# Kernel tuning notes

Measured on AMD Instinct MI355X. Metric: run time of the kernel, lower is better.

The kernel has to match this reference:

```python
import jax, jax.numpy as jnp
import numpy as np

B, C, D, H, W = 16, 8, 511, 16, 16
NHEADS = 16
DIM = C * H * W          # 2048 hidden size
SEQ = D + 1              # 512 tokens incl. cls
HEAD_DIM = DIM // NHEADS # 128


def setup_inputs() -> dict:
    key = jax.random.key(0)
    ks = jax.random.split(key, 8)
    s = 0.02  # weight init scale
    return {
        "x": jax.random.normal(ks[0], (B, C, D, H, W), jnp.float32),
        "pos_embedding": jax.random.normal(ks[1], (1, SEQ, DIM), jnp.float32),
        "cls": jax.random.normal(ks[2], (1, 1, DIM), jnp.float32),
        "qkv_w": jax.random.normal(ks[3], (DIM, 3 * DIM), jnp.float32) * s,
        "qkv_b": jnp.zeros((3 * DIM,), jnp.float32),
        "proj_w": jax.random.normal(ks[4], (DIM, DIM), jnp.float32) * s,
        "proj_b": jnp.zeros((DIM,), jnp.float32),
    }


def reference(x, pos_embedding, cls, qkv_w, qkv_b, proj_w, proj_b):
    b = x.shape[0]
    # rearrange 'b c d h w -> b d (c h w)'
    tok = jnp.transpose(x, (0, 2, 1, 3, 4)).reshape(b, D, DIM)
    tok = jnp.concatenate([jnp.broadcast_to(cls, (b, 1, DIM)), tok], axis=1)
    tok = tok + pos_embedding  # (b, SEQ, DIM)
    # qkv projection (dropout probs are 0 -> identity)
    qkv = tok @ qkv_w + qkv_b  # (b, SEQ, 3*DIM)
    qkv = qkv.reshape(b, SEQ, 3, NHEADS, HEAD_DIM).transpose(2, 0, 3, 1, 4)
    q, k, v = qkv[0], qkv[1], qkv[2]  # each (b, nH, SEQ, hd)
    scale = HEAD_DIM ** -0.5
    score = jax.nn.softmax(jnp.einsum('bhqd,bhkd->bhqk', q, k) * scale, axis=-1)
    out = jnp.einsum('bhqk,bhkd->bhqd', score, v)
    out = out.transpose(0, 2, 1, 3).reshape(b, SEQ, DIM)
    out = out @ proj_w + proj_b
    return out[:, 0]  # cls token, (b, DIM)
```

## Files before the change

### kernel.cpp

```cpp
#include <hip/hip_runtime.h>


#define BB   16
#define CC   8
#define DD   511
#define DIM  2048
#define SEQ  512
#define NH   16
#define HD   128
#define W3   6144
#define SCALE 0.08838834764831845f

#define Q_OFF   0
#define G_OFF   2048
#define AO_OFF  2064
#define SC_OFF  34832
#define ZERO_N  165904
#define R_OFF   165904
#define RB_OFF  198672
#define U_OFF   231440
#define POST_OFF 755728

#define PSTR 520

typedef __attribute__((ext_vector_type(8))) short short8;
typedef __attribute__((ext_vector_type(4))) float floatx4;

static __device__ inline short bf_hi(float f) {
  return (short)(__float_as_uint(f) >> 16);
}
static __device__ inline float bf_hif(float f) {
  return __uint_as_float(__float_as_uint(f) & 0xffff0000u);
}

__global__ __launch_bounds__(256) void k0_prep(
    const float* __restrict__ pos, float* __restrict__ ws,
    float* __restrict__ out) {
  int blk = blockIdx.x + blockIdx.y * 16;
  int t = threadIdx.x;
  for (int i = blk * 256 + t; i < ZERO_N; i += 1024 * 256) ws[i] = 0.f;
  for (int i = blk * 256 + t; i < BB * DIM; i += 1024 * 256) out[i] = 0.f;
  __shared__ float tile[32][33];
  int jt = blockIdx.x, dt = blockIdx.y;
  int tx = t & 31, ty = t >> 5;
#pragma unroll
  for (int r = 0; r < 32; r += 8)
    tile[ty + r][tx] = pos[(size_t)(jt * 32 + ty + r) * DIM + dt * 32 + tx];
  __syncthreads();
  float* pt = ws + POST_OFF;
#pragma unroll
  for (int r = 0; r < 32; r += 8)
    pt[(size_t)(dt * 32 + ty + r) * SEQ + jt * 32 + tx] = tile[tx][ty + r];
}

__global__ __launch_bounds__(256) void k1_q(
    const float* __restrict__ pos, const float* __restrict__ cls,
    const float* __restrict__ qkv_w, const float* __restrict__ qkv_b,
    float* __restrict__ ws) {
  int n  = blockIdx.x * 256 + threadIdx.x;
  int d0 = blockIdx.y * 32;
  float acc = (blockIdx.y == 0) ? qkv_b[n] : 0.f;
#pragma unroll 8
  for (int d = d0; d < d0 + 32; ++d) {
    float t0 = cls[d] + pos[d];
    acc += t0 * qkv_w[(size_t)d * W3 + n];
  }
  atomicAdd(&ws[Q_OFF + n], acc);
}

__global__ __launch_bounds__(128) void k2_r(
    const float* __restrict__ qkv_w, const float* __restrict__ pos,
    const float* __restrict__ cls, float* __restrict__ ws) {
  __shared__ float qs[HD];
  int h = blockIdx.y;
  int d = blockIdx.x * 128 + threadIdx.x;
  if (threadIdx.x < HD) qs[threadIdx.x] = ws[Q_OFF + h * HD + threadIdx.x];
  __syncthreads();
  const float4* w4 = reinterpret_cast<const float4*>(
      qkv_w + (size_t)d * W3 + DIM + h * HD);
  float acc = 0.f;
#pragma unroll 8
  for (int e4 = 0; e4 < 32; ++e4) {
    float4 w = w4[e4];
    acc += qs[e4*4+0]*w.x + qs[e4*4+1]*w.y + qs[e4*4+2]*w.z + qs[e4*4+3]*w.w;
  }
  float r = acc * SCALE;
  int i = h * DIM + d;
  ws[R_OFF + i] = r;
  short* rb = (short*)(ws + RB_OFF);
  rb[i] = bf_hi(r);
  rb[NH * DIM + i] = bf_hi(r - bf_hif(r));
  float g = (cls[d] + pos[d]) * r;
  for (int m = 1; m < 64; m <<= 1) g += __shfl_xor(g, m, 64);
  if ((threadIdx.x & 63) == 0) atomicAdd(&ws[G_OFF + h], g);
}

__global__ __launch_bounds__(256) void k3_scores_mfma(
    const float* __restrict__ x, const float* __restrict__ pos,
    float* __restrict__ ws) {
  int jt2 = blockIdx.x, b = blockIdx.y, ks = blockIdx.z;
  int t = threadIdx.x;
  int w = t >> 6, l = t & 63;
  int jt = jt2 * 4 + w;
  int m16 = l & 15, kg = l >> 4;
  int jrow = 1 + jt * 16 + m16;
  int jc = jrow < SEQ ? jrow : (SEQ - 1);
  const size_t xrow = (size_t)b * CC * DD * 256 + (size_t)(jc - 1) * 256;
  const short* rh = (const short*)(ws + RB_OFF);
  const short* rl = rh + NH * DIM;
  floatx4 acc = {0.f, 0.f, 0.f, 0.f};
#pragma unroll 2
  for (int kk = ks * 16; kk < ks * 16 + 16; ++kk) {
    int d0 = kk * 32 + kg * 8;
    int c = d0 >> 8, doff = d0 & 255;
    const float4* xp = reinterpret_cast<const float4*>(
        x + xrow + (size_t)c * DD * 256 + doff);
    const float4* pp = reinterpret_cast<const float4*>(
        pos + (size_t)jc * DIM + d0);
    float4 xa = xp[0], xb = xp[1];
    float4 pa = pp[0], pb = pp[1];
    float f[8] = {xa.x + pa.x, xa.y + pa.y, xa.z + pa.z, xa.w + pa.w,
                  xb.x + pb.x, xb.y + pb.y, xb.z + pb.z, xb.w + pb.w};
    short8 ahi, alo;
#pragma unroll
    for (int i = 0; i < 8; ++i) {
      ahi[i] = bf_hi(f[i]);
      alo[i] = bf_hi(f[i] - bf_hif(f[i]));
    }
    short8 bhi = *reinterpret_cast<const short8*>(rh + m16 * DIM + d0);
    short8 blo = *reinterpret_cast<const short8*>(rl + m16 * DIM + d0);
    acc = __builtin_amdgcn_mfma_f32_16x16x32_bf16(ahi, bhi, acc, 0, 0, 0);
    acc = __builtin_amdgcn_mfma_f32_16x16x32_bf16(ahi, blo, acc, 0, 0, 0);
    acc = __builtin_amdgcn_mfma_f32_16x16x32_bf16(alo, bhi, acc, 0, 0, 0);
  }
  int h = m16;
#pragma unroll
  for (int reg = 0; reg < 4; ++reg) {
    int row = kg * 4 + reg;
    int j = 1 + jt * 16 + row;
    if (j < SEQ)
      atomicAdd(&ws[SC_OFF + (size_t)(b * NH + h) * SEQ + j], acc[reg]);
  }
}

__global__ __launch_bounds__(256) void k5_pv_mfma(
    const float* __restrict__ x, const float* __restrict__ cls,
    float* __restrict__ ws) {
  int dt = blockIdx.x, b = blockIdx.y, t = threadIdx.x;
  __shared__ short phl[NH * PSTR];
  __shared__ short pll[NH * PSTR];
  int w = t >> 6, l = t & 63;
  for (int rr = 0; rr < 4; ++rr) {
    int h = w * 4 + rr;
    const float* sch = ws + SC_OFF + (size_t)(b * NH + h) * SEQ;
    float gam = ws[G_OFF + h];
    float s[8];
#pragma unroll
    for (int i = 0; i < 8; ++i) s[i] = sch[i * 64 + l];
    if (l == 0) s[0] = gam;
    float mx = s[0];
#pragma unroll
    for (int i = 1; i < 8; ++i) mx = fmaxf(mx, s[i]);
    for (int m = 1; m < 64; m <<= 1) mx = fmaxf(mx, __shfl_xor(mx, m, 64));
    float e[8], sum = 0.f;
#pragma unroll
    for (int i = 0; i < 8; ++i) { e[i] = __expf(s[i] - mx); sum += e[i]; }
    for (int m = 1; m < 64; m <<= 1) sum += __shfl_xor(sum, m, 64);
    float inv = 1.f / sum;
#pragma unroll
    for (int i = 0; i < 8; ++i) {
      float p = e[i] * inv;
      int j = i * 64 + l;
      phl[h * PSTR + j] = bf_hi(p);
      pll[h * PSTR + j] = bf_hi(p - bf_hif(p));
    }
  }
  __syncthreads();
  int m16 = l & 15, kq = l >> 4;
  int dcol = dt * 64 + w * 16 + m16;
  int c = dcol >> 8, doff = dcol & 255;
  const float* xcol = x + (size_t)b * CC * DD * 256 + (size_t)c * DD * 256 + doff;
  const float* ptcol = ws + POST_OFF + (size_t)dcol * SEQ;
  float clsv0 = cls[dcol];
  const short8* pph = reinterpret_cast<const short8*>(&phl[m16 * PSTR]);
  const short8* ppl = reinterpret_cast<const short8*>(&pll[m16 * PSTR]);
  floatx4 acc = {0.f, 0.f, 0.f, 0.f};
  for (int kk = 0; kk < 16; ++kk) {
    int jb = kk * 32 + kq * 8;
    const float* xp = xcol + ((size_t)jb - 1) * 256;
    const float* xp_safe = (jb == 0) ? xcol : xp;
    const float4* pt4 = reinterpret_cast<const float4*>(ptcol + jb);
    float4 pt0 = pt4[0], pt1 = pt4[1];
    float ptv[8] = {pt0.x, pt0.y, pt0.z, pt0.w, pt1.x, pt1.y, pt1.z, pt1.w};
    float f[8];
    float x0 = xp_safe[0];
    f[0] = ((jb == 0) ? clsv0 : x0) + ptv[0];
#pragma unroll
    for (int e = 1; e < 8; ++e)
      f[e] = xp[(size_t)e * 256] + ptv[e];
    short8 thi, tlo;
#pragma unroll
    for (int i = 0; i < 8; ++i) {
      thi[i] = bf_hi(f[i]);
      tlo[i] = bf_hi(f[i] - bf_hif(f[i]));
    }
    short8 phi = pph[kk * 4 + kq];
    short8 plo = ppl[kk * 4 + kq];
    acc = __builtin_amdgcn_mfma_f32_16x16x32_bf16(phi, thi, acc, 0, 0, 0);
    acc = __builtin_amdgcn_mfma_f32_16x16x32_bf16(phi, tlo, acc, 0, 0, 0);
    acc = __builtin_amdgcn_mfma_f32_16x16x32_bf16(plo, thi, acc, 0, 0, 0);
  }
  float* ub = ws + U_OFF + (size_t)b * NH * DIM + dcol;
#pragma unroll
  for (int reg = 0; reg < 4; ++reg) {
    int h = kq * 4 + reg;
    ub[(size_t)h * DIM] = acc[reg];
  }
}

__global__ __launch_bounds__(256) void k6_ao(
    const float* __restrict__ qkv_w, const float* __restrict__ qkv_b,
    float* __restrict__ ws) {
  int nt = blockIdx.x, dc = blockIdx.y, t = threadIdx.x;
  int m = nt * 256 + t;
  int h0 = nt * 2;
  int d0 = dc * 32;
  __shared__ float us[2][32][20];
  for (int i = t; i < 2 * 32 * BB; i += 256) {
    int dd = i & 31, b = (i >> 5) & 15, hh = i >> 9;
    us[hh][dd][b] = ws[U_OFF + (size_t)(b * NH + h0 + hh) * DIM + d0 + dd];
  }
  __syncthreads();
  int hl = t >> 7;
  float acc[BB];
#pragma unroll
  for (int b = 0; b < BB; ++b) acc[b] = 0.f;
  const float* wcol = qkv_w + (size_t)d0 * W3 + 2 * DIM + m;
#pragma unroll 4
  for (int dd = 0; dd < 32; ++dd) {
    float w = wcol[(size_t)dd * W3];
    const float4* u4 = reinterpret_cast<const float4*>(&us[hl][dd][0]);
    float4 u0 = u4[0], u1 = u4[1], u2 = u4[2], u3 = u4[3];
    acc[0]  += u0.x * w; acc[1]  += u0.y * w; acc[2]  += u0.z * w; acc[3]  += u0.w * w;
    acc[4]  += u1.x * w; acc[5]  += u1.y * w; acc[6]  += u1.z * w; acc[7]  += u1.w * w;
    acc[8]  += u2.x * w; acc[9]  += u2.y * w; acc[10] += u2.z * w; acc[11] += u2.w * w;
    acc[12] += u3.x * w; acc[13] += u3.y * w; acc[14] += u3.z * w; acc[15] += u3.w * w;
  }
  float bias = (dc == 0) ? qkv_b[2 * DIM + m] : 0.f;
#pragma unroll
  for (int b = 0; b < BB; ++b)
    atomicAdd(&ws[AO_OFF + b * DIM + m], acc[b] + bias);
}

__global__ __launch_bounds__(256) void k7_out(
    const float* __restrict__ proj_w, const float* __restrict__ proj_b,
    const float* __restrict__ ws, float* __restrict__ out) {
  int nt = blockIdx.x, mc = blockIdx.y, t = threadIdx.x;
  int n = nt * 256 + t;
  int m0 = mc * 32;
  __shared__ float as[32][20];
  for (int i = t; i < 32 * BB; i += 256) {
    int mm = i & 31, b = i >> 5;
    as[mm][b] = ws[AO_OFF + b * DIM + m0 + mm];
  }
  __syncthreads();
  float acc[BB];
#pragma unroll
  for (int b = 0; b < BB; ++b) acc[b] = 0.f;
  const float* wcol = proj_w + (size_t)m0 * DIM + n;
#pragma unroll 4
  for (int mm = 0; mm < 32; ++mm) {
    float w = wcol[(size_t)mm * DIM];
    const float4* a4 = reinterpret_cast<const float4*>(&as[mm][0]);
    float4 a0 = a4[0], a1 = a4[1], a2 = a4[2], a3 = a4[3];
    acc[0]  += a0.x * w; acc[1]  += a0.y * w; acc[2]  += a0.z * w; acc[3]  += a0.w * w;
    acc[4]  += a1.x * w; acc[5]  += a1.y * w; acc[6]  += a1.z * w; acc[7]  += a1.w * w;
    acc[8]  += a2.x * w; acc[9]  += a2.y * w; acc[10] += a2.z * w; acc[11] += a2.w * w;
    acc[12] += a3.x * w; acc[13] += a3.y * w; acc[14] += a3.z * w; acc[15] += a3.w * w;
  }
  float bias = (mc == 0) ? proj_b[n] : 0.f;
#pragma unroll
  for (int b = 0; b < BB; ++b)
    atomicAdd(&out[b * DIM + n], acc[b] + bias);
}

extern "C" void kernel_launch(void* const* d_in, const int* in_sizes, int n_in,
                              void* d_out, int out_size, void* d_ws, size_t ws_size,
                              hipStream_t stream) {
  const float* x      = (const float*)d_in[0];
  const float* pos    = (const float*)d_in[1];
  const float* cls    = (const float*)d_in[2];
  const float* qkv_w  = (const float*)d_in[3];
  const float* qkv_b  = (const float*)d_in[4];
  const float* proj_w = (const float*)d_in[5];
  const float* proj_b = (const float*)d_in[6];
  float* ws  = (float*)d_ws;
  float* out = (float*)d_out;

  k0_prep       <<<dim3(16, 64),    256, 0, stream>>>(pos, ws, out);
  k1_q          <<<dim3(8, 64),     256, 0, stream>>>(pos, cls, qkv_w, qkv_b, ws);
  k2_r          <<<dim3(16, 16),    128, 0, stream>>>(qkv_w, pos, cls, ws);
  k3_scores_mfma<<<dim3(8, 16, 4),  256, 0, stream>>>(x, pos, ws);
  k5_pv_mfma    <<<dim3(32, 16),    256, 0, stream>>>(x, cls, ws);
  k6_ao         <<<dim3(8, 64),     256, 0, stream>>>(qkv_w, qkv_b, ws);
  k7_out        <<<dim3(8, 64),     256, 0, stream>>>(proj_w, proj_b, ws, out);
}
```

Baseline: 220.8 us.

## Drop prep kernel, replace atomics with partial buffers, stage PV tokens in LDS

Removes the prep kernel that zeroed workspace and transposed pos. The q projection and the score kernel now write per-split partial results that are summed by their consumers instead of accumulating with atomics, and the zeroing of the remaining atomic targets moves into k1. The PV kernel now loads x+pos tiles with coalesced float4 reads, converts them to bf16 hi/lo pairs into double-buffered LDS, and reads MFMA operands from there, replacing strided per-column global loads. The cost is extra partial-sum reads, more LDS use and a barrier every iteration.

```diff
diff --git a/kernel.cpp b/kernel.cpp
--- a/kernel.cpp
+++ b/kernel.cpp
@@ -11,17 +11,18 @@
 #define W3   6144
 #define SCALE 0.08838834764831845f
 
-#define Q_OFF   0
-#define G_OFF   2048
-#define AO_OFF  2064
-#define SC_OFF  34832
-#define ZERO_N  165904
-#define R_OFF   165904
-#define RB_OFF  198672
-#define U_OFF   231440
-#define POST_OFF 755728
+#define QP_OFF  0
+#define G_OFF   131072
+#define AO_OFF  131088
+#define SCP_OFF 163856
+#define SCPSZ   131072
+#define R_OFF   688144
+#define RB_OFF  720912
+#define U_OFF   753680
 
 #define PSTR 520
+#define CJ   32
+#define TSTR 68
 
 typedef __attribute__((ext_vector_type(8))) short short8;
 typedef __attribute__((ext_vector_type(4))) float floatx4;
@@ -31,41 +32,25 @@
 }
 static __device__ inline float bf_hif(float f) {
   return __uint_as_float(__float_as_uint(f) & 0xffff0000u);
-}
-
-__global__ __launch_bounds__(256) void k0_prep(
-    const float* __restrict__ pos, float* __restrict__ ws,
-    float* __restrict__ out) {
-  int blk = blockIdx.x + blockIdx.y * 16;
-  int t = threadIdx.x;
-  for (int i = blk * 256 + t; i < ZERO_N; i += 1024 * 256) ws[i] = 0.f;
-  for (int i = blk * 256 + t; i < BB * DIM; i += 1024 * 256) out[i] = 0.f;
-  __shared__ float tile[32][33];
-  int jt = blockIdx.x, dt = blockIdx.y;
-  int tx = t & 31, ty = t >> 5;
-#pragma unroll
-  for (int r = 0; r < 32; r += 8)
-    tile[ty + r][tx] = pos[(size_t)(jt * 32 + ty + r) * DIM + dt * 32 + tx];
-  __syncthreads();
-  float* pt = ws + POST_OFF;
-#pragma unroll
-  for (int r = 0; r < 32; r += 8)
-    pt[(size_t)(dt * 32 + ty + r) * SEQ + jt * 32 + tx] = tile[tx][ty + r];
 }
 
 __global__ __launch_bounds__(256) void k1_q(
     const float* __restrict__ pos, const float* __restrict__ cls,
     const float* __restrict__ qkv_w, const float* __restrict__ qkv_b,
-    float* __restrict__ ws) {
+    float* __restrict__ ws, float* __restrict__ out) {
   int n  = blockIdx.x * 256 + threadIdx.x;
-  int d0 = blockIdx.y * 32;
-  float acc = (blockIdx.y == 0) ? qkv_b[n] : 0.f;
+  int dc = blockIdx.y;
+  int tid = (blockIdx.x + blockIdx.y * 8) * 256 + threadIdx.x;
+  if (tid < 32784) ws[G_OFF + tid] = 0.f;
+  if (tid < BB * DIM) out[tid] = 0.f;
+  int d0 = dc * 32;
+  float acc = (dc == 0) ? qkv_b[n] : 0.f;
 #pragma unroll 8
   for (int d = d0; d < d0 + 32; ++d) {
     float t0 = cls[d] + pos[d];
     acc += t0 * qkv_w[(size_t)d * W3 + n];
   }
-  atomicAdd(&ws[Q_OFF + n], acc);
+  ws[QP_OFF + dc * DIM + n] = acc;
 }
 
 __global__ __launch_bounds__(128) void k2_r(
@@ -74,7 +59,11 @@
   __shared__ float qs[HD];
   int h = blockIdx.y;
   int d = blockIdx.x * 128 + threadIdx.x;
-  if (threadIdx.x < HD) qs[threadIdx.x] = ws[Q_OFF + h * HD + threadIdx.x];
+  float qa = 0.f;
+#pragma unroll 8
+  for (int c = 0; c < 64; ++c)
+    qa += ws[QP_OFF + c * DIM + h * HD + threadIdx.x];
+  qs[threadIdx.x] = qa;
   __syncthreads();
   const float4* w4 = reinterpret_cast<const float4*>(
       qkv_w + (size_t)d * W3 + DIM + h * HD);
@@ -139,24 +128,30 @@
     int row = kg * 4 + reg;
     int j = 1 + jt * 16 + row;
     if (j < SEQ)
-      atomicAdd(&ws[SC_OFF + (size_t)(b * NH + h) * SEQ + j], acc[reg]);
+      ws[SCP_OFF + (size_t)ks * SCPSZ + (size_t)(b * NH + h) * SEQ + j] =
+          acc[reg];
   }
 }
 
 __global__ __launch_bounds__(256) void k5_pv_mfma(
-    const float* __restrict__ x, const float* __restrict__ cls,
-    float* __restrict__ ws) {
+    const float* __restrict__ x, const float* __restrict__ pos,
+    const float* __restrict__ cls, float* __restrict__ ws) {
   int dt = blockIdx.x, b = blockIdx.y, t = threadIdx.x;
-  __shared__ short phl[NH * PSTR];
-  __shared__ short pll[NH * PSTR];
+  __shared__ __attribute__((aligned(16))) short phl[NH * PSTR];
+  __shared__ __attribute__((aligned(16))) short pll[NH * PSTR];
+  __shared__ short ths[2][CJ][TSTR];
+  __shared__ short tls[2][CJ][TSTR];
   int w = t >> 6, l = t & 63;
   for (int rr = 0; rr < 4; ++rr) {
     int h = w * 4 + rr;
-    const float* sch = ws + SC_OFF + (size_t)(b * NH + h) * SEQ;
+    const float* sc0 = ws + SCP_OFF + (size_t)(b * NH + h) * SEQ;
     float gam = ws[G_OFF + h];
     float s[8];
 #pragma unroll
-    for (int i = 0; i < 8; ++i) s[i] = sch[i * 64 + l];
+    for (int i = 0; i < 8; ++i) {
+      int j = i * 64 + l;
+      s[i] = sc0[j] + sc0[SCPSZ + j] + sc0[2 * SCPSZ + j] + sc0[3 * SCPSZ + j];
+    }
     if (l == 0) s[0] = gam;
     float mx = s[0];
 #pragma unroll
@@ -175,34 +170,47 @@
       pll[h * PSTR + j] = bf_hi(p - bf_hif(p));
     }
   }
-  __syncthreads();
+  const size_t xb = (size_t)b * CC * DD * 256;
+  auto stage = [&](int kk, int buf) {
+#pragma unroll
+    for (int rep = 0; rep < 2; ++rep) {
+      int idx = rep * 256 + t;
+      int jj = idx >> 4, f4 = idx & 15;
+      int j = kk * CJ + jj;
+      int dbase = dt * 64 + f4 * 4;
+      float4 pv = *reinterpret_cast<const float4*>(pos + (size_t)j * DIM + dbase);
+      float4 xv;
+      if (j == 0) {
+        xv = *reinterpret_cast<const float4*>(cls + dbase);
+      } else {
+        int c = dbase >> 8, doff = dbase & 255;
+        xv = *reinterpret_cast<const float4*>(
+            x + xb + (size_t)c * DD * 256 + (size_t)(j - 1) * 256 + doff);
+      }
+      float f[4] = {xv.x + pv.x, xv.y + pv.y, xv.z + pv.z, xv.w + pv.w};
+#pragma unroll
+      for (int k = 0; k < 4; ++k) {
+        ths[buf][jj][f4 * 4 + k] = bf_hi(f[k]);
+        tls[buf][jj][f4 * 4 + k] = bf_hi(f[k] - bf_hif(f[k]));
+      }
+    }
+  };
+  stage(0, 0);
   int m16 = l & 15, kq = l >> 4;
-  int dcol = dt * 64 + w * 16 + m16;
-  int c = dcol >> 8, doff = dcol & 255;
-  const float* xcol = x + (size_t)b * CC * DD * 256 + (size_t)c * DD * 256 + doff;
-  const float* ptcol = ws + POST_OFF + (size_t)dcol * SEQ;
-  float clsv0 = cls[dcol];
+  int wd = w * 16 + m16;
+  int dcol = dt * 64 + wd;
   const short8* pph = reinterpret_cast<const short8*>(&phl[m16 * PSTR]);
   const short8* ppl = reinterpret_cast<const short8*>(&pll[m16 * PSTR]);
   floatx4 acc = {0.f, 0.f, 0.f, 0.f};
   for (int kk = 0; kk < 16; ++kk) {
-    int jb = kk * 32 + kq * 8;
-    const float* xp = xcol + ((size_t)jb - 1) * 256;
-    const float* xp_safe = (jb == 0) ? xcol : xp;
-    const float4* pt4 = reinterpret_cast<const float4*>(ptcol + jb);
-    float4 pt0 = pt4[0], pt1 = pt4[1];
-    float ptv[8] = {pt0.x, pt0.y, pt0.z, pt0.w, pt1.x, pt1.y, pt1.z, pt1.w};
-    float f[8];
-    float x0 = xp_safe[0];
-    f[0] = ((jb == 0) ? clsv0 : x0) + ptv[0];
-#pragma unroll
-    for (int e = 1; e < 8; ++e)
-      f[e] = xp[(size_t)e * 256] + ptv[e];
+    __syncthreads();
+    if (kk < 15) stage(kk + 1, (kk + 1) & 1);
+    int buf = kk & 1;
     short8 thi, tlo;
 #pragma unroll
     for (int i = 0; i < 8; ++i) {
-      thi[i] = bf_hi(f[i]);
-      tlo[i] = bf_hi(f[i] - bf_hif(f[i]));
+      thi[i] = ths[buf][kq * 8 + i][wd];
+      tlo[i] = tls[buf][kq * 8 + i][wd];
     }
     short8 phi = pph[kk * 4 + kq];
     short8 plo = ppl[kk * 4 + kq];
@@ -212,10 +220,8 @@
   }
   float* ub = ws + U_OFF + (size_t)b * NH * DIM + dcol;
 #pragma unroll
-  for (int reg = 0; reg < 4; ++reg) {
-    int h = kq * 4 + reg;
-    ub[(size_t)h * DIM] = acc[reg];
-  }
+  for (int reg = 0; reg < 4; ++reg)
+    ub[(size_t)(kq * 4 + reg) * DIM] = acc[reg];
 }
 
 __global__ __launch_bounds__(256) void k6_ao(
@@ -297,11 +303,10 @@
   float* ws  = (float*)d_ws;
   float* out = (float*)d_out;
 
-  k0_prep       <<<dim3(16, 64),    256, 0, stream>>>(pos, ws, out);
-  k1_q          <<<dim3(8, 64),     256, 0, stream>>>(pos, cls, qkv_w, qkv_b, ws);
+  k1_q          <<<dim3(8, 64),     256, 0, stream>>>(pos, cls, qkv_w, qkv_b, ws, out);
   k2_r          <<<dim3(16, 16),    128, 0, stream>>>(qkv_w, pos, cls, ws);
   k3_scores_mfma<<<dim3(8, 16, 4),  256, 0, stream>>>(x, pos, ws);
-  k5_pv_mfma    <<<dim3(32, 16),    256, 0, stream>>>(x, cls, ws);
+  k5_pv_mfma    <<<dim3(32, 16),    256, 0, stream>>>(x, pos, cls, ws);
   k6_ao         <<<dim3(8, 64),     256, 0, stream>>>(qkv_w, qkv_b, ws);
   k7_out        <<<dim3(8, 64),     256, 0, stream>>>(proj_w, proj_b, ws, out);
 }
```

Result: no change. 221.5 us (+0.3%).
